# Kernel optimization log

Hardware: AMD Instinct MI355X
Metric: run time of the kernel (lower is better)

Reference implementation:

```python
import jax, jax.numpy as jnp
import numpy as np

NEG_INF = -1.0e9  # value used by masked_fill in the original

def setup_inputs() -> dict:
    key = jax.random.key(0)
    kq, kk, kv, km = jax.random.split(key, 4)
    B, H, S, D = 2, 16, 2048, 64
    query = jax.random.normal(kq, (B, H, S, D), dtype=jnp.float32)
    key_t = jax.random.normal(kk, (B, H, S, D), dtype=jnp.float32)
    value = jax.random.normal(kv, (B, H, S, D), dtype=jnp.float32)
    mask = jax.random.randint(km, (1, 1, S, S), 0, 2, dtype=jnp.int32)
    return {"query": query, "key": key_t, "value": value, "mask": mask}

def reference(query, key, value, mask):
    d_k = query.shape[-1]
    # scores: [B,H,Sq,Sk]
    scores = jnp.einsum("bhqd,bhkd->bhqk", query, key) / jnp.sqrt(jnp.float32(d_k))
    scores = jnp.where(mask == 0, jnp.float32(NEG_INF), scores)
    attn = jax.nn.softmax(scores, axis=-1)
    out = jnp.einsum("bhqk,bhkd->bhqd", attn, value)
    return (out, attn)
```

## Files before the change

### kernel.cpp

```cpp
#include <hip/hip_runtime.h>


#define S_LEN 2048
#define D_DIM 64
#define BH_N  32
#define NELEM (BH_N*S_LEN*D_DIM)

typedef __bf16 bf16;
typedef bf16 bf16x4 __attribute__((ext_vector_type(4)));
typedef bf16 bf16x8 __attribute__((ext_vector_type(8)));
typedef float f32x4 __attribute__((ext_vector_type(4)));

__device__ __attribute__((aligned(16))) bf16 g_Qb[NELEM];
__device__ __attribute__((aligned(16))) bf16 g_Kb[NELEM];
__device__ __attribute__((aligned(16))) bf16 g_VT[NELEM];
__device__ unsigned long long g_bits[S_LEN*S_LEN/64];

__global__ void cvt_qk_kernel(const float* __restrict__ Qs, const float* __restrict__ Ks){
  int i = blockIdx.x*256 + threadIdx.x;
  float4 q = reinterpret_cast<const float4*>(Qs)[i];
  float4 k = reinterpret_cast<const float4*>(Ks)[i];
  bf16x4 oq = {(bf16)q.x,(bf16)q.y,(bf16)q.z,(bf16)q.w};
  bf16x4 ok = {(bf16)k.x,(bf16)k.y,(bf16)k.z,(bf16)k.w};
  ((bf16x4*)g_Qb)[i] = oq;
  ((bf16x4*)g_Kb)[i] = ok;
}

__global__ void transpose_v_kernel(const float* __restrict__ V){
  __shared__ float sv[64][65];
  int bh = blockIdx.x >> 5;
  int k0 = (blockIdx.x & 31) << 6;
  const float* src = V + ((size_t)bh*S_LEN + k0)*D_DIM;
  #pragma unroll
  for (int i=0;i<16;i++){
    int e = threadIdx.x + i*256;
    sv[e>>6][e&63] = src[e];
  }
  __syncthreads();
  bf16* dst = g_VT + (size_t)bh*D_DIM*S_LEN + k0;
  #pragma unroll
  for (int i=0;i<16;i++){
    int e = threadIdx.x + i*256;
    int d = e>>6, k = e&63;
    dst[(size_t)d*S_LEN + k] = (bf16)sv[k][d];
  }
}

__global__ void build_bits_kernel(const int* __restrict__ mask){
  int gid = blockIdx.x*256 + threadIdx.x;
  unsigned long long b = __ballot(mask[gid] != 0);
  if ((threadIdx.x & 63) == 0) g_bits[gid >> 6] = b;
}

__global__ __launch_bounds__(256, 4)
void attn_main_kernel(float* __restrict__ out, float* __restrict__ attn){
  __shared__ bf16 sQ [64][72];
  __shared__ bf16 sK [64][72];
  __shared__ bf16 sVT[64][72];
  __shared__ bf16 sP [64][72];

  const int tid  = threadIdx.x;
  const int wave = tid >> 6, lane = tid & 63;
  const int quad = lane >> 4, l16 = lane & 15;
  const int bh = blockIdx.x >> 5, qb = blockIdx.x & 31;
  const int q0 = qb << 6, m0 = wave << 4;

  const bf16* __restrict__ Qh  = g_Qb + ((size_t)bh*S_LEN + q0)*D_DIM;
  const bf16* __restrict__ Kh  = g_Kb + (size_t)bh*S_LEN*D_DIM;
  const bf16* __restrict__ VTh = g_VT + (size_t)bh*D_DIM*S_LEN;
  float* __restrict__ outh  = out  + ((size_t)bh*S_LEN + q0)*D_DIM;
  float* __restrict__ attnh = attn + (size_t)bh*S_LEN*S_LEN + (size_t)q0*S_LEN;

  #pragma unroll
  for (int i=0;i<2;i++){
    int e = tid + i*256; int r = e>>3, c = (e&7)*8;
    *(bf16x8*)&sQ[r][c] = *(const bf16x8*)&Qh[r*D_DIM + c];
  }
  __syncthreads();

  const bf16x8 aq0 = *(const bf16x8*)&sQ[m0 + l16][quad*8];
  const bf16x8 aq1 = *(const bf16x8*)&sQ[m0 + l16][32 + quad*8];

  float lp[4] = {0.f,0.f,0.f,0.f};
  f32x4 oacc[4];
  #pragma unroll
  for (int n=0;n<4;n++) oacc[n] = (f32x4){0.f,0.f,0.f,0.f};

  const int mrow = q0 + m0 + quad*4;

  for (int kt=0; kt<32; ++kt){
    const bf16* __restrict__ Ksrc = Kh + (size_t)(kt<<6)*D_DIM;
    #pragma unroll
    for (int i=0;i<2;i++){
      int e = tid + i*256; int r = e>>3, c = (e&7)*8;
      *(bf16x8*)&sK[r][c] = *(const bf16x8*)&Ksrc[r*D_DIM + c];
    }
    #pragma unroll
    for (int i=0;i<2;i++){
      int e = tid + i*256; int d = e>>3, c = (e&7)*8;
      *(bf16x8*)&sVT[d][c] = *(const bf16x8*)&VTh[(size_t)d*S_LEN + (kt<<6) + c];
    }
    __syncthreads();

    unsigned long long wr[4];
    #pragma unroll
    for (int r=0;r<4;r++) wr[r] = g_bits[(size_t)(mrow + r)*32 + kt];

    #pragma unroll
    for (int n=0;n<4;n++){
      bf16x8 bk0 = *(const bf16x8*)&sK[n*16 + l16][quad*8];
      bf16x8 bk1 = *(const bf16x8*)&sK[n*16 + l16][32 + quad*8];
      f32x4 c = (f32x4){0.f,0.f,0.f,0.f};
      c = __builtin_amdgcn_mfma_f32_16x16x32_bf16(aq0, bk0, c, 0,0,0);
      c = __builtin_amdgcn_mfma_f32_16x16x32_bf16(aq1, bk1, c, 0,0,0);
      int shift = n*16 + l16;
      #pragma unroll
      for (int r=0;r<4;r++){
        float p = ((wr[r] >> shift) & 1ull) ? __expf(c[r]*0.125f) : 0.f;
        lp[r] += p;
        sP[m0 + quad*4 + r][shift] = (bf16)p;
      }
    }

    #pragma unroll
    for (int s=0;s<2;s++){
      bf16x8 pa = *(const bf16x8*)&sP[m0 + l16][s*32 + quad*8];
      #pragma unroll
      for (int n=0;n<4;n++){
        bf16x8 vb = *(const bf16x8*)&sVT[n*16 + l16][s*32 + quad*8];
        oacc[n] = __builtin_amdgcn_mfma_f32_16x16x32_bf16(pa, vb, oacc[n], 0,0,0);
      }
    }
    __syncthreads();
  }

  #pragma unroll
  for (int r=0;r<4;r++){
    float v = lp[r];
    #pragma unroll
    for (int off=1; off<16; off<<=1) v += __shfl_xor(v, off);
    lp[r] = 1.0f / v;
  }

  #pragma unroll
  for (int n=0;n<4;n++){
    #pragma unroll
    for (int r=0;r<4;r++)
      outh[(size_t)(m0 + quad*4 + r)*D_DIM + n*16 + l16] = oacc[n][r] * lp[r];
  }

  for (int kt=0; kt<32; ++kt){
    const bf16* __restrict__ Ksrc = Kh + (size_t)(kt<<6)*D_DIM;
    __syncthreads();
    #pragma unroll
    for (int i=0;i<2;i++){
      int e = tid + i*256; int r = e>>3, c = (e&7)*8;
      *(bf16x8*)&sK[r][c] = *(const bf16x8*)&Ksrc[r*D_DIM + c];
    }
    __syncthreads();

    unsigned long long wr[4];
    #pragma unroll
    for (int r=0;r<4;r++) wr[r] = g_bits[(size_t)(mrow + r)*32 + kt];

    #pragma unroll
    for (int n=0;n<4;n++){
      bf16x8 bk0 = *(const bf16x8*)&sK[n*16 + l16][quad*8];
      bf16x8 bk1 = *(const bf16x8*)&sK[n*16 + l16][32 + quad*8];
      f32x4 c = (f32x4){0.f,0.f,0.f,0.f};
      c = __builtin_amdgcn_mfma_f32_16x16x32_bf16(aq0, bk0, c, 0,0,0);
      c = __builtin_amdgcn_mfma_f32_16x16x32_bf16(aq1, bk1, c, 0,0,0);
      int shift = n*16 + l16;
      #pragma unroll
      for (int r=0;r<4;r++){
        float a = ((wr[r] >> shift) & 1ull) ? __expf(c[r]*0.125f)*lp[r] : 0.f;
        attnh[(size_t)(m0 + quad*4 + r)*S_LEN + (kt<<6) + shift] = a;
      }
    }
  }
}

extern "C" void kernel_launch(void* const* d_in, const int* in_sizes, int n_in,
                              void* d_out, int out_size, void* d_ws, size_t ws_size,
                              hipStream_t stream){
  (void)in_sizes; (void)n_in; (void)d_ws; (void)ws_size; (void)out_size;
  const float* Q    = (const float*)d_in[0];
  const float* K    = (const float*)d_in[1];
  const float* V    = (const float*)d_in[2];
  const int*   mask = (const int*)d_in[3];
  float* out  = (float*)d_out;
  float* attn = out + (size_t)NELEM;

  cvt_qk_kernel     <<<NELEM/4/256,        256, 0, stream>>>(Q, K);
  transpose_v_kernel<<<BH_N*(S_LEN/64),    256, 0, stream>>>(V);
  build_bits_kernel <<<S_LEN*S_LEN/256,    256, 0, stream>>>(mask);
  attn_main_kernel  <<<BH_N*(S_LEN/64),    256, 0, stream>>>(out, attn);
}
```

Measured before the change: 701.5 us.

## Drop LDS staging of Q/K/V, use exp2 softmax and nontemporal output stores

Each wave now reads its Q, K and V^T fragments straight from global memory (via cache) instead of staging them in shared memory. This removes the per-tile barriers and LDS traffic, leaving only the P tile in shared memory. The exponent becomes a single exp2 with a folded 0.125*log2(e) scale. The second pass folds the 1/sum normalisation into the exponent as a log2 offset. Output and attention stores are nontemporal to avoid polluting cache with the large attention write, at the risk of redundant per-wave global loads of K/V.

After: 895.9 us. 1.28x slower.

```diff
diff --git a/kernel.cpp b/kernel.cpp
--- a/kernel.cpp
+++ b/kernel.cpp
@@ -10,6 +10,8 @@
 typedef bf16 bf16x4 __attribute__((ext_vector_type(4)));
 typedef bf16 bf16x8 __attribute__((ext_vector_type(8)));
 typedef float f32x4 __attribute__((ext_vector_type(4)));
+
+#define K1 0.1803368801111244f
 
 __device__ __attribute__((aligned(16))) bf16 g_Qb[NELEM];
 __device__ __attribute__((aligned(16))) bf16 g_Kb[NELEM];
@@ -54,10 +56,7 @@
 
 __global__ __launch_bounds__(256, 4)
 void attn_main_kernel(float* __restrict__ out, float* __restrict__ attn){
-  __shared__ bf16 sQ [64][72];
-  __shared__ bf16 sK [64][72];
-  __shared__ bf16 sVT[64][72];
-  __shared__ bf16 sP [64][72];
+  __shared__ bf16 sP[64][72];
 
   const int tid  = threadIdx.x;
   const int wave = tid >> 6, lane = tid & 63;
@@ -65,21 +64,14 @@
   const int bh = blockIdx.x >> 5, qb = blockIdx.x & 31;
   const int q0 = qb << 6, m0 = wave << 4;
 
-  const bf16* __restrict__ Qh  = g_Qb + ((size_t)bh*S_LEN + q0)*D_DIM;
   const bf16* __restrict__ Kh  = g_Kb + (size_t)bh*S_LEN*D_DIM;
   const bf16* __restrict__ VTh = g_VT + (size_t)bh*D_DIM*S_LEN;
   float* __restrict__ outh  = out  + ((size_t)bh*S_LEN + q0)*D_DIM;
   float* __restrict__ attnh = attn + (size_t)bh*S_LEN*S_LEN + (size_t)q0*S_LEN;
 
-  #pragma unroll
-  for (int i=0;i<2;i++){
-    int e = tid + i*256; int r = e>>3, c = (e&7)*8;
-    *(bf16x8*)&sQ[r][c] = *(const bf16x8*)&Qh[r*D_DIM + c];
-  }
-  __syncthreads();
-
-  const bf16x8 aq0 = *(const bf16x8*)&sQ[m0 + l16][quad*8];
-  const bf16x8 aq1 = *(const bf16x8*)&sQ[m0 + l16][32 + quad*8];
+  const bf16* qr = g_Qb + ((size_t)bh*S_LEN + q0 + m0 + l16)*D_DIM + quad*8;
+  const bf16x8 aq0 = *(const bf16x8*)qr;
+  const bf16x8 aq1 = *(const bf16x8*)(qr + 32);
 
   float lp[4] = {0.f,0.f,0.f,0.f};
   f32x4 oacc[4];
@@ -89,18 +81,7 @@
   const int mrow = q0 + m0 + quad*4;
 
   for (int kt=0; kt<32; ++kt){
-    const bf16* __restrict__ Ksrc = Kh + (size_t)(kt<<6)*D_DIM;
-    #pragma unroll
-    for (int i=0;i<2;i++){
-      int e = tid + i*256; int r = e>>3, c = (e&7)*8;
-      *(bf16x8*)&sK[r][c] = *(const bf16x8*)&Ksrc[r*D_DIM + c];
-    }
-    #pragma unroll
-    for (int i=0;i<2;i++){
-      int e = tid + i*256; int d = e>>3, c = (e&7)*8;
-      *(bf16x8*)&sVT[d][c] = *(const bf16x8*)&VTh[(size_t)d*S_LEN + (kt<<6) + c];
-    }
-    __syncthreads();
+    const bf16* __restrict__ Kt = Kh + (size_t)(kt<<6)*D_DIM;
 
     unsigned long long wr[4];
     #pragma unroll
@@ -108,56 +89,53 @@
 
     #pragma unroll
     for (int n=0;n<4;n++){
-      bf16x8 bk0 = *(const bf16x8*)&sK[n*16 + l16][quad*8];
-      bf16x8 bk1 = *(const bf16x8*)&sK[n*16 + l16][32 + quad*8];
+      const bf16* kr = Kt + (n*16 + l16)*D_DIM + quad*8;
+      bf16x8 bk0 = *(const bf16x8*)kr;
+      bf16x8 bk1 = *(const bf16x8*)(kr + 32);
       f32x4 c = (f32x4){0.f,0.f,0.f,0.f};
       c = __builtin_amdgcn_mfma_f32_16x16x32_bf16(aq0, bk0, c, 0,0,0);
       c = __builtin_amdgcn_mfma_f32_16x16x32_bf16(aq1, bk1, c, 0,0,0);
       int shift = n*16 + l16;
       #pragma unroll
       for (int r=0;r<4;r++){
-        float p = ((wr[r] >> shift) & 1ull) ? __expf(c[r]*0.125f) : 0.f;
+        float p = ((wr[r] >> shift) & 1ull) ? __builtin_amdgcn_exp2f(c[r]*K1) : 0.f;
         lp[r] += p;
         sP[m0 + quad*4 + r][shift] = (bf16)p;
       }
     }
 
+    const bf16* Vt = VTh + (kt<<6);
     #pragma unroll
     for (int s=0;s<2;s++){
       bf16x8 pa = *(const bf16x8*)&sP[m0 + l16][s*32 + quad*8];
       #pragma unroll
       for (int n=0;n<4;n++){
-        bf16x8 vb = *(const bf16x8*)&sVT[n*16 + l16][s*32 + quad*8];
+        bf16x8 vb = *(const bf16x8*)(Vt + (size_t)(n*16 + l16)*S_LEN + s*32 + quad*8);
         oacc[n] = __builtin_amdgcn_mfma_f32_16x16x32_bf16(pa, vb, oacc[n], 0,0,0);
       }
     }
-    __syncthreads();
   }
 
+  float llp[4];
   #pragma unroll
   for (int r=0;r<4;r++){
     float v = lp[r];
     #pragma unroll
     for (int off=1; off<16; off<<=1) v += __shfl_xor(v, off);
-    lp[r] = 1.0f / v;
+    lp[r]  = 1.0f / v;
+    llp[r] = -__builtin_amdgcn_logf(v);
   }
 
   #pragma unroll
   for (int n=0;n<4;n++){
     #pragma unroll
     for (int r=0;r<4;r++)
-      outh[(size_t)(m0 + quad*4 + r)*D_DIM + n*16 + l16] = oacc[n][r] * lp[r];
+      __builtin_nontemporal_store(oacc[n][r]*lp[r],
+          &outh[(size_t)(m0 + quad*4 + r)*D_DIM + n*16 + l16]);
   }
 
   for (int kt=0; kt<32; ++kt){
-    const bf16* __restrict__ Ksrc = Kh + (size_t)(kt<<6)*D_DIM;
-    __syncthreads();
-    #pragma unroll
-    for (int i=0;i<2;i++){
-      int e = tid + i*256; int r = e>>3, c = (e&7)*8;
-      *(bf16x8*)&sK[r][c] = *(const bf16x8*)&Ksrc[r*D_DIM + c];
-    }
-    __syncthreads();
+    const bf16* __restrict__ Kt = Kh + (size_t)(kt<<6)*D_DIM;
 
     unsigned long long wr[4];
     #pragma unroll
@@ -165,16 +143,19 @@
 
     #pragma unroll
     for (int n=0;n<4;n++){
-      bf16x8 bk0 = *(const bf16x8*)&sK[n*16 + l16][quad*8];
-      bf16x8 bk1 = *(const bf16x8*)&sK[n*16 + l16][32 + quad*8];
+      const bf16* kr = Kt + (n*16 + l16)*D_DIM + quad*8;
+      bf16x8 bk0 = *(const bf16x8*)kr;
+      bf16x8 bk1 = *(const bf16x8*)(kr + 32);
       f32x4 c = (f32x4){0.f,0.f,0.f,0.f};
       c = __builtin_amdgcn_mfma_f32_16x16x32_bf16(aq0, bk0, c, 0,0,0);
       c = __builtin_amdgcn_mfma_f32_16x16x32_bf16(aq1, bk1, c, 0,0,0);
       int shift = n*16 + l16;
       #pragma unroll
       for (int r=0;r<4;r++){
-        float a = ((wr[r] >> shift) & 1ull) ? __expf(c[r]*0.125f)*lp[r] : 0.f;
-        attnh[(size_t)(m0 + quad*4 + r)*S_LEN + (kt<<6) + shift] = a;
+        float a = ((wr[r] >> shift) & 1ull)
+                    ? __builtin_amdgcn_exp2f(__builtin_fmaf(c[r], K1, llp[r])) : 0.f;
+        __builtin_nontemporal_store(a,
+            &attnh[(size_t)(m0 + quad*4 + r)*S_LEN + (kt<<6) + shift]);
       }
     }
   }
```
